# Optimization experiments

Measured on AMD Instinct MI355X. Metric: run time of the kernel, lower is better.

## Reference

```python
import jax, jax.numpy as jnp
import numpy as np

B, DIM, H, W = 8, 96, 256, 256
NH, WS, SS = 3, 8, 4
HD = DIM // NH
SCALE = HD ** -0.5
N = WS * WS  # tokens per window


def _rel_pos_log(ws):
    # [N, N, 2] signed log relative coordinates (matches get_relative_positions)
    coords = np.stack(np.meshgrid(np.arange(ws), np.arange(ws), indexing='ij'))
    cf = coords.reshape(2, -1)
    rel = (cf[:, :, None] - cf[:, None, :]).transpose(1, 2, 0).astype(np.float32)
    return np.sign(rel) * np.log1p(np.abs(rel))


def _attn_mask(Hh, Ww, ws, ss):
    # Swin shifted-window mask: [nW, N, N] with 0 / -100
    img = np.zeros((Hh, Ww))
    cnt = 0
    sl = (slice(0, -ws), slice(-ws, -ss), slice(-ss, None))
    for h in sl:
        for w in sl:
            img[h, w] = cnt
            cnt += 1
    mw = img.reshape(Hh // ws, ws, Ww // ws, ws).transpose(0, 2, 1, 3).reshape(-1, ws * ws)
    am = mw[:, None, :] - mw[:, :, None]
    return np.where(am != 0, -100.0, 0.0).astype(np.float32)


REL_POS = jnp.asarray(_rel_pos_log(WS))        # [N, N, 2]
ATTN_MASK = jnp.asarray(_attn_mask(H, W, WS, SS))  # [nW, N, N]


def setup_inputs() -> dict:
    key = jax.random.key(0)
    ks = jax.random.split(key, 8)
    s = 0.02
    return {
        'x': jax.random.normal(ks[0], (B, DIM, H, W), jnp.float32),
        'V_w': jax.random.normal(ks[1], (DIM, DIM), jnp.float32) * s,
        'V_b': jnp.zeros((DIM,), jnp.float32),
        'QK_w': jax.random.normal(ks[2], (2 * DIM, DIM), jnp.float32) * s,
        'QK_b': jnp.zeros((2 * DIM,), jnp.float32),
        'proj_w': jax.random.normal(ks[3], (DIM, DIM), jnp.float32) * s,
        'proj_b': jnp.zeros((DIM,), jnp.float32),
        'dw_w': jax.random.normal(ks[4], (DIM, 5, 5), jnp.float32) * s,
        'dw_b': jnp.zeros((DIM,), jnp.float32),
        'meta_w1': jax.random.normal(ks[5], (256, 2), jnp.float32) * 0.1,
        'meta_b1': jnp.zeros((256,), jnp.float32),
        'meta_w2': jax.random.normal(ks[6], (NH, 256), jnp.float32) * 0.1,
        'meta_b2': jnp.zeros((NH,), jnp.float32),
    }


def reference(x, V_w, V_b, QK_w, QK_b, proj_w, proj_b, dw_w, dw_b,
              meta_w1, meta_b1, meta_w2, meta_b2):
    # 1x1 convs as channel matmuls
    V = jnp.einsum('bchw,oc->bohw', x, V_w) + V_b[None, :, None, None]
    QK = jnp.einsum('bchw,oc->bohw', x, QK_w) + QK_b[None, :, None, None]
    qkv = jnp.concatenate([QK, V], axis=1).transpose(0, 2, 3, 1)  # [B,H,W,3C]
    # cyclic shift
    qkv = jnp.roll(qkv, (-SS, -SS), axis=(1, 2))
    # window partition -> [B*nW, N, 3C]
    xw = qkv.reshape(B, H // WS, WS, W // WS, WS, 3 * DIM)
    xw = xw.transpose(0, 1, 3, 2, 4, 5).reshape(-1, N, 3 * DIM)
    qkv3 = xw.reshape(-1, N, 3, NH, HD).transpose(2, 0, 3, 1, 4)  # [3, B_, nh, N, hd]
    q, k, v = qkv3[0] * SCALE, qkv3[1], qkv3[2]
    attn = jnp.einsum('whnd,whmd->whnm', q, k)  # [B_, nh, N, N]
    # MLP relative-position bias
    bias = jax.nn.relu(REL_POS @ meta_w1.T + meta_b1) @ meta_w2.T + meta_b2  # [N,N,nh]
    attn = attn + bias.transpose(2, 0, 1)[None]
    nW = ATTN_MASK.shape[0]
    attn = attn.reshape(B, nW, NH, N, N) + ATTN_MASK[None, :, None]
    attn = jax.nn.softmax(attn, axis=-1).reshape(-1, NH, N, N)
    xo = jnp.einsum('whnm,whmd->wnhd', attn, v).reshape(-1, N, DIM)
    # window reverse -> [B,H,W,C]
    xr = xo.reshape(B, H // WS, W // WS, WS, WS, DIM)
    xr = xr.transpose(0, 1, 3, 2, 4, 5).reshape(B, H, W, DIM)
    xr = jnp.roll(xr, (SS, SS), axis=(1, 2)).transpose(0, 3, 1, 2)  # [B,C,H,W]
    # depthwise 5x5 conv with reflect padding on V
    Vp = jnp.pad(V, ((0, 0), (0, 0), (2, 2), (2, 2)), mode='reflect')
    conv_out = jax.lax.conv_general_dilated(
        Vp, dw_w.reshape(DIM, 1, 5, 5), (1, 1), 'VALID',
        feature_group_count=DIM,
        dimension_numbers=('NCHW', 'OIHW', 'NCHW')) + dw_b[None, :, None, None]
    out = jnp.einsum('bchw,oc->bohw', conv_out + xr, proj_w) + proj_b[None, :, None, None]
    return out
```

## Files before the change

kernel.cpp:

```cpp
#include <hip/hip_runtime.h>
#include <hip/hip_bf16.h>

#define HW 65536
#define SCALE_Q 0.17677669529663687f

typedef __bf16 bf16x8 __attribute__((ext_vector_type(8)));
typedef float f32x4 __attribute__((ext_vector_type(4)));

__global__ void bias_kernel(const float* __restrict__ w1, const float* __restrict__ b1,
                            const float* __restrict__ w2, const float* __restrict__ b2,
                            float* __restrict__ biasF) {
    int gid = blockIdx.x * blockDim.x + threadIdx.x;
    if (gid >= 12288) return;
    int lane = gid & 63, r = (gid >> 6) & 3, ni = (gid >> 8) & 3, mi = (gid >> 10) & 3, h = gid >> 12;
    int i = mi * 16 + ((lane >> 4) << 2) + r;
    int j = ni * 16 + (lane & 15);
    float di = (float)((i >> 3) - (j >> 3));
    float dj = (float)((i & 7) - (j & 7));
    float r0 = (di > 0.f ? 1.f : (di < 0.f ? -1.f : 0.f)) * log1pf(fabsf(di));
    float r1 = (dj > 0.f ? 1.f : (dj < 0.f ? -1.f : 0.f)) * log1pf(fabsf(dj));
    float acc = 0.f;
    for (int t = 0; t < 256; ++t) {
        float u = fmaf(w1[2 * t], r0, fmaf(w1[2 * t + 1], r1, b1[t]));
        u = fmaxf(u, 0.f);
        acc = fmaf(w2[h * 256 + t], u, acc);
    }
    biasF[gid] = acc + b2[h];
}

__global__ void wtrans_kernel(const float* __restrict__ QK_w, const float* __restrict__ V_w,
                              const float* __restrict__ proj_w,
                              __bf16* __restrict__ Whi, __bf16* __restrict__ Wlo,
                              __bf16* __restrict__ WpHi, __bf16* __restrict__ WpLo) {
    int idx = blockIdx.x * blockDim.x + threadIdx.x;
    if (idx < 288 * 96) {
        int oo = idx / 96, c = idx - oo * 96;
        int h = oo / 96, rem = oo - h * 96, grp = rem >> 5, d = rem & 31;
        float w = (grp == 0) ? QK_w[(h * 32 + d) * 96 + c]
                : (grp == 1) ? QK_w[(96 + h * 32 + d) * 96 + c]
                             : V_w[(h * 32 + d) * 96 + c];
        __bf16 hi = (__bf16)w;
        Whi[idx] = hi;
        Wlo[idx] = (__bf16)(w - (float)hi);
    } else if (idx < 288 * 96 + 96 * 96) {
        int rdx = idx - 288 * 96;
        float w = proj_w[rdx];
        __bf16 hi = (__bf16)w;
        WpHi[rdx] = hi;
        WpLo[rdx] = (__bf16)(w - (float)hi);
    }
}

__global__ __launch_bounds__(256, 3) void fused_qkv_attn(
    const float* __restrict__ x,
    const __bf16* __restrict__ Whi, const __bf16* __restrict__ Wlo,
    const float* __restrict__ QK_b, const float* __restrict__ V_b,
    const float* __restrict__ biasF,
    unsigned short* __restrict__ Vout, float* __restrict__ xr) {
    __shared__ __align__(16) char lds[53376];
    int tid = threadIdx.x;
    int w4 = tid >> 6;
    int lane = tid & 63;
    int l16 = lane & 15;
    int g8 = (lane >> 4) << 3;
    int g4 = (lane >> 4) << 2;
    int bx0 = blockIdx.x;
    int bxs = (bx0 & 7) * 256 + (bx0 >> 3);
    int b = bxs >> 8;
    int wh = (bxs >> 3) & 31;
    int ww0 = (bxs & 7) << 2;
    int wh8 = wh << 3;
    int wb8 = ww0 << 3;
    int ww = ww0 + w4;
    int ti = lane >> 3, tj = lane & 7;
    int ph = (wh8 + ti + 4) & 255;
    int pw = ((ww << 3) + tj + 4) & 255;
    int pos   = ph * 256 + pw;
    int pos_s = (wh8 + ti) * 256 + (ww << 3) + tj;

    __bf16* Xh = (__bf16*)lds;
    const float* xb = x + (size_t)b * 96 * HW;
    for (int idx = tid; idx < 24576; idx += 256) {
        int c = idx >> 8, r = (idx >> 5) & 7, col = idx & 31;
        int pph = (wh8 + r + 4) & 255;
        int ppw = (wb8 + col + 4) & 255;
        Xh[(col >> 3) * 6672 + (r * 8 + (col & 7)) * 104 + c] =
            (__bf16)xb[(size_t)c * HW + pph * 256 + ppw];
    }
    __syncthreads();

    bf16x8 Ah[4][3];
    const __bf16* Xw = Xh + w4 * 6672;
#pragma unroll
    for (int mi = 0; mi < 4; ++mi)
#pragma unroll
        for (int ks = 0; ks < 3; ++ks)
            Ah[mi][ks] = *(const bf16x8*)(Xw + (mi * 16 + l16) * 104 + ks * 32 + g8);
    __syncthreads();

    char* hb = lds + w4 * 9984;
    __bf16* slab = (__bf16*)hb;
    __bf16* Vt   = (__bf16*)(hb + 5120);
    float*  Xr   = (float*)hb;

    bool bhh = (wh == 31), bww = (ww == 31);
    int rc[4];
#pragma unroll
    for (int ni = 0; ni < 4; ++ni) {
        int t = ni * 16 + l16;
        rc[ni] = (bhh ? (((t >> 3) < 4) ? 1 : 2) : 0) * 3 + (bww ? (((t & 7) < 4) ? 1 : 2) : 0);
    }

#pragma unroll 1
    for (int h = 0; h < 3; ++h) {
        bf16x8 Qf[4], Kf[4];
        {
            f32x4 acc[4][2];
#pragma unroll
            for (int mi = 0; mi < 4; ++mi)
#pragma unroll
                for (int ni = 0; ni < 2; ++ni) acc[mi][ni] = (f32x4){0.f, 0.f, 0.f, 0.f};
#pragma unroll
            for (int ks = 0; ks < 3; ++ks)
#pragma unroll
                for (int ni = 0; ni < 2; ++ni) {
                    bf16x8 Bh = *(const bf16x8*)(Whi + (h * 96 + ni * 16 + l16) * 96 + ks * 32 + g8);
#pragma unroll
                    for (int mi = 0; mi < 4; ++mi)
                        acc[mi][ni] = __builtin_amdgcn_mfma_f32_16x16x32_bf16(Ah[mi][ks], Bh, acc[mi][ni], 0, 0, 0);
                }
#pragma unroll
            for (int ni = 0; ni < 2; ++ni) {
                float bias = QK_b[h * 32 + ni * 16 + l16];
#pragma unroll
                for (int mi = 0; mi < 4; ++mi)
#pragma unroll
                    for (int r = 0; r < 4; ++r)
                        slab[(mi * 16 + g4 + r) * 40 + ni * 16 + l16] = (__bf16)((acc[mi][ni][r] + bias) * SCALE_Q);
            }
#pragma unroll
            for (int mi = 0; mi < 4; ++mi) Qf[mi] = *(const bf16x8*)(slab + (mi * 16 + l16) * 40 + g8);
        }
        {
            f32x4 acc[4][2];
#pragma unroll
            for (int mi = 0; mi < 4; ++mi)
#pragma unroll
                for (int ni = 0; ni < 2; ++ni) acc[mi][ni] = (f32x4){0.f, 0.f, 0.f, 0.f};
#pragma unroll
            for (int ks = 0; ks < 3; ++ks)
#pragma unroll
                for (int ni = 0; ni < 2; ++ni) {
                    bf16x8 Bh = *(const bf16x8*)(Whi + (h * 96 + 32 + ni * 16 + l16) * 96 + ks * 32 + g8);
#pragma unroll
                    for (int mi = 0; mi < 4; ++mi)
                        acc[mi][ni] = __builtin_amdgcn_mfma_f32_16x16x32_bf16(Ah[mi][ks], Bh, acc[mi][ni], 0, 0, 0);
                }
#pragma unroll
            for (int ni = 0; ni < 2; ++ni) {
                float bias = QK_b[96 + h * 32 + ni * 16 + l16];
#pragma unroll
                for (int mi = 0; mi < 4; ++mi)
#pragma unroll
                    for (int r = 0; r < 4; ++r)
                        slab[(mi * 16 + g4 + r) * 40 + ni * 16 + l16] = (__bf16)(acc[mi][ni][r] + bias);
            }
#pragma unroll
            for (int mi = 0; mi < 4; ++mi) Kf[mi] = *(const bf16x8*)(slab + (mi * 16 + l16) * 40 + g8);
        }
        {
            f32x4 acc[4][2];
#pragma unroll
            for (int mi = 0; mi < 4; ++mi)
#pragma unroll
                for (int ni = 0; ni < 2; ++ni) acc[mi][ni] = (f32x4){0.f, 0.f, 0.f, 0.f};
#pragma unroll
            for (int ks = 0; ks < 3; ++ks)
#pragma unroll
                for (int ni = 0; ni < 2; ++ni) {
                    int oo = (h * 96 + 64 + ni * 16 + l16) * 96 + ks * 32 + g8;
                    bf16x8 Bh = *(const bf16x8*)(Whi + oo);
                    bf16x8 Bl = *(const bf16x8*)(Wlo + oo);
#pragma unroll
                    for (int mi = 0; mi < 4; ++mi) {
                        acc[mi][ni] = __builtin_amdgcn_mfma_f32_16x16x32_bf16(Ah[mi][ks], Bh, acc[mi][ni], 0, 0, 0);
                        acc[mi][ni] = __builtin_amdgcn_mfma_f32_16x16x32_bf16(Ah[mi][ks], Bl, acc[mi][ni], 0, 0, 0);
                    }
                }
#pragma unroll
            for (int ni = 0; ni < 2; ++ni) {
                float bias = V_b[h * 32 + ni * 16 + l16];
#pragma unroll
                for (int mi = 0; mi < 4; ++mi)
#pragma unroll
                    for (int r = 0; r < 4; ++r)
                        Vt[(ni * 16 + l16) * 72 + mi * 16 + g4 + r] = (__bf16)(acc[mi][ni][r] + bias);
            }
        }
#pragma unroll
        for (int d = 0; d < 32; ++d)
            Vout[(size_t)(b * 96 + h * 32 + d) * HW + pos_s] = ((const unsigned short*)Vt)[d * 72 + lane];

        f32x4 sc[4][4];
#pragma unroll
        for (int mi = 0; mi < 4; ++mi)
#pragma unroll
            for (int ni = 0; ni < 4; ++ni) {
                sc[mi][ni] = (f32x4){0.f, 0.f, 0.f, 0.f};
                sc[mi][ni] = __builtin_amdgcn_mfma_f32_16x16x32_bf16(Qf[mi], Kf[ni], sc[mi][ni], 0, 0, 0);
            }
        const float* bF = biasF + h * 4096;
#pragma unroll
        for (int mi = 0; mi < 4; ++mi)
#pragma unroll
            for (int r = 0; r < 4; ++r) {
                int row = mi * 16 + g4 + r;
                float s0 = sc[mi][0][r] + bF[((mi * 4 + 0) * 4 + r) * 64 + lane];
                float s1 = sc[mi][1][r] + bF[((mi * 4 + 1) * 4 + r) * 64 + lane];
                float s2 = sc[mi][2][r] + bF[((mi * 4 + 2) * 4 + r) * 64 + lane];
                float s3 = sc[mi][3][r] + bF[((mi * 4 + 3) * 4 + r) * 64 + lane];
                if (bhh || bww) {
                    int rr = (bhh ? (((row >> 3) < 4) ? 1 : 2) : 0) * 3 +
                             (bww ? (((row & 7) < 4) ? 1 : 2) : 0);
                    if (rr != rc[0]) s0 -= 100.f;
                    if (rr != rc[1]) s1 -= 100.f;
                    if (rr != rc[2]) s2 -= 100.f;
                    if (rr != rc[3]) s3 -= 100.f;
                }
                float mm = fmaxf(fmaxf(s0, s1), fmaxf(s2, s3));
                mm = fmaxf(mm, __shfl_xor(mm, 1));
                mm = fmaxf(mm, __shfl_xor(mm, 2));
                mm = fmaxf(mm, __shfl_xor(mm, 4));
                mm = fmaxf(mm, __shfl_xor(mm, 8));
                float e0 = __expf(s0 - mm), e1 = __expf(s1 - mm);
                float e2 = __expf(s2 - mm), e3 = __expf(s3 - mm);
                float sum = e0 + e1 + e2 + e3;
                sum += __shfl_xor(sum, 1);
                sum += __shfl_xor(sum, 2);
                sum += __shfl_xor(sum, 4);
                sum += __shfl_xor(sum, 8);
                float inv = 1.f / sum;
                sc[mi][0][r] = e0 * inv;
                sc[mi][1][r] = e1 * inv;
                sc[mi][2][r] = e2 * inv;
                sc[mi][3][r] = e3 * inv;
            }
        f32x4 po[4][2];
#pragma unroll
        for (int mi = 0; mi < 4; ++mi)
#pragma unroll
            for (int ni = 0; ni < 2; ++ni) po[mi][ni] = (f32x4){0.f, 0.f, 0.f, 0.f};
#pragma unroll
        for (int ks = 0; ks < 2; ++ks) {
#pragma unroll
            for (int mi = 0; mi < 4; ++mi)
#pragma unroll
                for (int r = 0; r < 4; ++r) {
                    int row = mi * 16 + g4 + r;
                    slab[row * 40 + l16]      = (__bf16)sc[mi][ks * 2 + 0][r];
                    slab[row * 40 + 16 + l16] = (__bf16)sc[mi][ks * 2 + 1][r];
                }
            bf16x8 Vf[2], Pf;
#pragma unroll
            for (int ni = 0; ni < 2; ++ni)
                Vf[ni] = *(const bf16x8*)(Vt + (ni * 16 + l16) * 72 + ks * 32 + g8);
#pragma unroll
            for (int mi = 0; mi < 4; ++mi) {
                Pf = *(const bf16x8*)(slab + (mi * 16 + l16) * 40 + g8);
#pragma unroll
                for (int ni = 0; ni < 2; ++ni)
                    po[mi][ni] = __builtin_amdgcn_mfma_f32_16x16x32_bf16(Pf, Vf[ni], po[mi][ni], 0, 0, 0);
            }
        }
#pragma unroll
        for (int mi = 0; mi < 4; ++mi)
#pragma unroll
            for (int ni = 0; ni < 2; ++ni)
#pragma unroll
                for (int r = 0; r < 4; ++r)
                    Xr[(mi * 16 + g4 + r) * 36 + ni * 16 + l16] = po[mi][ni][r];
        float* xrg = xr + (size_t)(b * 96 + h * 32) * HW + pos;
#pragma unroll
        for (int c4 = 0; c4 < 8; ++c4) {
            f32x4 v = *(const f32x4*)(Xr + lane * 36 + c4 * 4);
            xrg[(size_t)(c4 * 4 + 0) * HW] = v[0];
            xrg[(size_t)(c4 * 4 + 1) * HW] = v[1];
            xrg[(size_t)(c4 * 4 + 2) * HW] = v[2];
            xrg[(size_t)(c4 * 4 + 3) * HW] = v[3];
        }
    }
}

__global__ __launch_bounds__(256) void dwproj_kernel(
    const __hip_bfloat16* __restrict__ Vs, const float* __restrict__ dw_w,
    const float* __restrict__ dw_b, const __bf16* __restrict__ WpHi,
    const __bf16* __restrict__ WpLo, const float* __restrict__ pb,
    float* __restrict__ T) {
    __shared__ __align__(16) __bf16 Ts[13312];
    int bx0 = blockIdx.x;
    int bx = (bx0 & 7) * 512 + (bx0 >> 3);
    int half = bx & 1, h = (bx >> 1) & 255, b = bx >> 9;
    int w0 = half << 7;
    int tid = threadIdx.x;
    for (int task = tid; task < 1536; task += 256) {
        int c = task >> 4, g = task & 15;
        int wbase = w0 + (g << 3);
        const __hip_bfloat16* Vp = Vs + (size_t)(b * 96 + c) * HW;
        const float* wt = dw_w + c * 25;
        float acc[8];
        float bias = dw_b[c];
#pragma unroll
        for (int i = 0; i < 8; ++i) acc[i] = bias;
        bool fast = (wbase >= 8) && (wbase <= 240);
#pragma unroll
        for (int dy = -2; dy <= 2; ++dy) {
            int hh = h + dy;
            hh = hh < 0 ? -hh : (hh > 255 ? 510 - hh : hh);
            int hs = (hh + 252) & 255;
            const __hip_bfloat16* row = Vp + hs * 256;
            float xv[12];
            if (fast) {
                const uint* rp = (const uint*)(row + (wbase - 6));
#pragma unroll
                for (int g2 = 0; g2 < 6; ++g2) {
                    uint u = rp[g2];
                    xv[2 * g2]     = __uint_as_float(u << 16);
                    xv[2 * g2 + 1] = __uint_as_float(u & 0xffff0000u);
                }
            } else {
#pragma unroll
                for (int idx = 0; idx < 12; ++idx) {
                    int cw = wbase - 2 + idx;
                    cw = cw < 0 ? -cw : (cw > 255 ? 510 - cw : cw);
                    int cs = (cw + 252) & 255;
                    uint u = *(const unsigned short*)(row + cs);
                    xv[idx] = __uint_as_float(u << 16);
                }
            }
            const float* w5 = wt + (dy + 2) * 5;
#pragma unroll
            for (int dx = 0; dx < 5; ++dx) {
                float wv = w5[dx];
#pragma unroll
                for (int i = 0; i < 8; ++i) acc[i] = fmaf(wv, xv[i + dx], acc[i]);
            }
        }
        const float* xp = T + (size_t)(b * 96 + c) * HW + h * 256;
        f32x4 x0 = *(const f32x4*)(xp + wbase);
        f32x4 x1 = *(const f32x4*)(xp + wbase + 4);
#pragma unroll
        for (int i = 0; i < 4; ++i) { acc[i] += x0[i]; acc[4 + i] += x1[i]; }
#pragma unroll
        for (int i = 0; i < 8; ++i) Ts[(g * 8 + i) * 104 + c] = (__bf16)acc[i];
    }
    __syncthreads();
    int lane = tid & 63;
    int l16 = lane & 15;
    int g8 = (lane >> 4) << 3;
    int g4 = (lane >> 4) << 2;
    int wv = tid >> 6;
    f32x4 po[2][6];
#pragma unroll
    for (int mi = 0; mi < 2; ++mi)
#pragma unroll
        for (int ni = 0; ni < 6; ++ni) po[mi][ni] = (f32x4){0.f, 0.f, 0.f, 0.f};
#pragma unroll
    for (int ks = 0; ks < 3; ++ks) {
        bf16x8 Av[2];
#pragma unroll
        for (int mi = 0; mi < 2; ++mi)
            Av[mi] = *(const bf16x8*)(Ts + (wv * 32 + mi * 16 + l16) * 104 + ks * 32 + g8);
#pragma unroll
        for (int ni = 0; ni < 6; ++ni) {
            int o = ni * 16 + l16;
            bf16x8 Bh = *(const bf16x8*)(WpHi + o * 96 + ks * 32 + g8);
            bf16x8 Bl = *(const bf16x8*)(WpLo + o * 96 + ks * 32 + g8);
#pragma unroll
            for (int mi = 0; mi < 2; ++mi) {
                po[mi][ni] = __builtin_amdgcn_mfma_f32_16x16x32_bf16(Av[mi], Bh, po[mi][ni], 0, 0, 0);
                po[mi][ni] = __builtin_amdgcn_mfma_f32_16x16x32_bf16(Av[mi], Bl, po[mi][ni], 0, 0, 0);
            }
        }
    }
#pragma unroll
    for (int ni = 0; ni < 6; ++ni) {
        int o = ni * 16 + l16;
        float bias = pb[o];
#pragma unroll
        for (int mi = 0; mi < 2; ++mi) {
            f32x4 v = po[mi][ni];
            v[0] += bias; v[1] += bias; v[2] += bias; v[3] += bias;
            *(f32x4*)(T + (size_t)(b * 96 + o) * HW + h * 256 + w0 + wv * 32 + mi * 16 + g4) = v;
        }
    }
}

extern "C" void kernel_launch(void* const* d_in, const int* in_sizes, int n_in,
                              void* d_out, int out_size, void* d_ws, size_t ws_size,
                              hipStream_t stream) {
    const float* x      = (const float*)d_in[0];
    const float* V_w    = (const float*)d_in[1];
    const float* V_b    = (const float*)d_in[2];
    const float* QK_w   = (const float*)d_in[3];
    const float* QK_b   = (const float*)d_in[4];
    const float* proj_w = (const float*)d_in[5];
    const float* proj_b = (const float*)d_in[6];
    const float* dw_w   = (const float*)d_in[7];
    const float* dw_b   = (const float*)d_in[8];
    const float* mw1    = (const float*)d_in[9];
    const float* mb1    = (const float*)d_in[10];
    const float* mw2    = (const float*)d_in[11];
    const float* mb2    = (const float*)d_in[12];
    float* out = (float*)d_out;

    char* ws = (char*)d_ws;
    __hip_bfloat16* Vbuf = (__hip_bfloat16*)ws;
    float*  biasF = (float*)(ws + 100663296);
    __bf16* Whi   = (__bf16*)(ws + 100663296 + 49152);
    __bf16* Wlo   = (__bf16*)(ws + 100663296 + 49152 + 55296);
    __bf16* WpHi  = (__bf16*)(ws + 100663296 + 49152 + 2 * 55296);
    __bf16* WpLo  = (__bf16*)(ws + 100663296 + 49152 + 2 * 55296 + 18432);

    bias_kernel<<<48, 256, 0, stream>>>(mw1, mb1, mw2, mb2, biasF);
    wtrans_kernel<<<144, 256, 0, stream>>>(QK_w, V_w, proj_w, Whi, Wlo, WpHi, WpLo);
    fused_qkv_attn<<<2048, 256, 0, stream>>>(x, Whi, Wlo, QK_b, V_b, biasF,
                                             (unsigned short*)Vbuf, out);
    dwproj_kernel<<<4096, 256, 0, stream>>>(Vbuf, dw_w, dw_b, WpHi, WpLo, proj_b, out);
}
```

Baseline: 710.5 us.

## Store attention output intermediate as bf16 and raise wave priority around MFMA blocks

The attention kernel now writes its windowed output to a separate bf16 workspace buffer instead of fp32 into the output tensor, and the depthwise/projection kernel reads it back as packed bf16. This halves the traffic for that intermediate in both the write and the read. It also wraps MFMA loops in s_setprio to favour matrix issue. It costs extra precision loss on the attention branch. The bf16 path is only taken when the workspace is large enough.

```diff
diff --git a/kernel.cpp b/kernel.cpp
--- a/kernel.cpp
+++ b/kernel.cpp
@@ -51,12 +51,13 @@
     }
 }
 
+template <bool XRB>
 __global__ __launch_bounds__(256, 3) void fused_qkv_attn(
     const float* __restrict__ x,
     const __bf16* __restrict__ Whi, const __bf16* __restrict__ Wlo,
     const float* __restrict__ QK_b, const float* __restrict__ V_b,
     const float* __restrict__ biasF,
-    unsigned short* __restrict__ Vout, float* __restrict__ xr) {
+    unsigned short* __restrict__ Vout, void* __restrict__ xrv) {
     __shared__ __align__(16) char lds[53376];
     int tid = threadIdx.x;
     int w4 = tid >> 6;
@@ -120,6 +121,7 @@
             for (int mi = 0; mi < 4; ++mi)
 #pragma unroll
                 for (int ni = 0; ni < 2; ++ni) acc[mi][ni] = (f32x4){0.f, 0.f, 0.f, 0.f};
+            __builtin_amdgcn_s_setprio(1);
 #pragma unroll
             for (int ks = 0; ks < 3; ++ks)
 #pragma unroll
@@ -129,6 +131,7 @@
                     for (int mi = 0; mi < 4; ++mi)
                         acc[mi][ni] = __builtin_amdgcn_mfma_f32_16x16x32_bf16(Ah[mi][ks], Bh, acc[mi][ni], 0, 0, 0);
                 }
+            __builtin_amdgcn_s_setprio(0);
 #pragma unroll
             for (int ni = 0; ni < 2; ++ni) {
                 float bias = QK_b[h * 32 + ni * 16 + l16];
@@ -147,6 +150,7 @@
             for (int mi = 0; mi < 4; ++mi)
 #pragma unroll
                 for (int ni = 0; ni < 2; ++ni) acc[mi][ni] = (f32x4){0.f, 0.f, 0.f, 0.f};
+            __builtin_amdgcn_s_setprio(1);
 #pragma unroll
             for (int ks = 0; ks < 3; ++ks)
 #pragma unroll
@@ -156,6 +160,7 @@
                     for (int mi = 0; mi < 4; ++mi)
                         acc[mi][ni] = __builtin_amdgcn_mfma_f32_16x16x32_bf16(Ah[mi][ks], Bh, acc[mi][ni], 0, 0, 0);
                 }
+            __builtin_amdgcn_s_setprio(0);
 #pragma unroll
             for (int ni = 0; ni < 2; ++ni) {
                 float bias = QK_b[96 + h * 32 + ni * 16 + l16];
@@ -174,6 +179,7 @@
             for (int mi = 0; mi < 4; ++mi)
 #pragma unroll
                 for (int ni = 0; ni < 2; ++ni) acc[mi][ni] = (f32x4){0.f, 0.f, 0.f, 0.f};
+            __builtin_amdgcn_s_setprio(1);
 #pragma unroll
             for (int ks = 0; ks < 3; ++ks)
 #pragma unroll
@@ -187,6 +193,7 @@
                         acc[mi][ni] = __builtin_amdgcn_mfma_f32_16x16x32_bf16(Ah[mi][ks], Bl, acc[mi][ni], 0, 0, 0);
                     }
                 }
+            __builtin_amdgcn_s_setprio(0);
 #pragma unroll
             for (int ni = 0; ni < 2; ++ni) {
                 float bias = V_b[h * 32 + ni * 16 + l16];
@@ -202,6 +209,7 @@
             Vout[(size_t)(b * 96 + h * 32 + d) * HW + pos_s] = ((const unsigned short*)Vt)[d * 72 + lane];
 
         f32x4 sc[4][4];
+        __builtin_amdgcn_s_setprio(1);
 #pragma unroll
         for (int mi = 0; mi < 4; ++mi)
 #pragma unroll
@@ -209,6 +217,7 @@
                 sc[mi][ni] = (f32x4){0.f, 0.f, 0.f, 0.f};
                 sc[mi][ni] = __builtin_amdgcn_mfma_f32_16x16x32_bf16(Qf[mi], Kf[ni], sc[mi][ni], 0, 0, 0);
             }
+        __builtin_amdgcn_s_setprio(0);
         const float* bF = biasF + h * 4096;
 #pragma unroll
         for (int mi = 0; mi < 4; ++mi)
@@ -264,6 +273,7 @@
 #pragma unroll
             for (int ni = 0; ni < 2; ++ni)
                 Vf[ni] = *(const bf16x8*)(Vt + (ni * 16 + l16) * 72 + ks * 32 + g8);
+            __builtin_amdgcn_s_setprio(1);
 #pragma unroll
             for (int mi = 0; mi < 4; ++mi) {
                 Pf = *(const bf16x8*)(slab + (mi * 16 + l16) * 40 + g8);
@@ -271,6 +281,7 @@
                 for (int ni = 0; ni < 2; ++ni)
                     po[mi][ni] = __builtin_amdgcn_mfma_f32_16x16x32_bf16(Pf, Vf[ni], po[mi][ni], 0, 0, 0);
             }
+            __builtin_amdgcn_s_setprio(0);
         }
 #pragma unroll
         for (int mi = 0; mi < 4; ++mi)
@@ -279,23 +290,37 @@
 #pragma unroll
                 for (int r = 0; r < 4; ++r)
                     Xr[(mi * 16 + g4 + r) * 36 + ni * 16 + l16] = po[mi][ni][r];
-        float* xrg = xr + (size_t)(b * 96 + h * 32) * HW + pos;
-#pragma unroll
-        for (int c4 = 0; c4 < 8; ++c4) {
-            f32x4 v = *(const f32x4*)(Xr + lane * 36 + c4 * 4);
-            xrg[(size_t)(c4 * 4 + 0) * HW] = v[0];
-            xrg[(size_t)(c4 * 4 + 1) * HW] = v[1];
-            xrg[(size_t)(c4 * 4 + 2) * HW] = v[2];
-            xrg[(size_t)(c4 * 4 + 3) * HW] = v[3];
+        if constexpr (XRB) {
+            unsigned short* xrg = (unsigned short*)xrv + (size_t)(b * 96 + h * 32) * HW + pos;
+#pragma unroll
+            for (int c4 = 0; c4 < 8; ++c4) {
+                f32x4 v = *(const f32x4*)(Xr + lane * 36 + c4 * 4);
+#pragma unroll
+                for (int j = 0; j < 4; ++j) {
+                    __bf16 t = (__bf16)v[j];
+                    xrg[(size_t)(c4 * 4 + j) * HW] = *(unsigned short*)&t;
+                }
+            }
+        } else {
+            float* xrg = (float*)xrv + (size_t)(b * 96 + h * 32) * HW + pos;
+#pragma unroll
+            for (int c4 = 0; c4 < 8; ++c4) {
+                f32x4 v = *(const f32x4*)(Xr + lane * 36 + c4 * 4);
+                xrg[(size_t)(c4 * 4 + 0) * HW] = v[0];
+                xrg[(size_t)(c4 * 4 + 1) * HW] = v[1];
+                xrg[(size_t)(c4 * 4 + 2) * HW] = v[2];
+                xrg[(size_t)(c4 * 4 + 3) * HW] = v[3];
+            }
         }
     }
 }
 
+template <bool XRB>
 __global__ __launch_bounds__(256) void dwproj_kernel(
     const __hip_bfloat16* __restrict__ Vs, const float* __restrict__ dw_w,
     const float* __restrict__ dw_b, const __bf16* __restrict__ WpHi,
     const __bf16* __restrict__ WpLo, const float* __restrict__ pb,
-    float* __restrict__ T) {
+    const void* __restrict__ xrv, float* __restrict__ T) {
     __shared__ __align__(16) __bf16 Ts[13312];
     int bx0 = blockIdx.x;
     int bx = (bx0 & 7) * 512 + (bx0 >> 3);
@@ -345,11 +370,24 @@
                 for (int i = 0; i < 8; ++i) acc[i] = fmaf(wv, xv[i + dx], acc[i]);
             }
         }
-        const float* xp = T + (size_t)(b * 96 + c) * HW + h * 256;
-        f32x4 x0 = *(const f32x4*)(xp + wbase);
-        f32x4 x1 = *(const f32x4*)(xp + wbase + 4);
-#pragma unroll
-        for (int i = 0; i < 4; ++i) { acc[i] += x0[i]; acc[4 + i] += x1[i]; }
+        if constexpr (XRB) {
+            const unsigned short* xp = (const unsigned short*)xrv + (size_t)(b * 96 + c) * HW + h * 256 + wbase;
+            uint4 u = *(const uint4*)xp;
+            acc[0] += __uint_as_float(u.x << 16);
+            acc[1] += __uint_as_float(u.x & 0xffff0000u);
+            acc[2] += __uint_as_float(u.y << 16);
+            acc[3] += __uint_as_float(u.y & 0xffff0000u);
+            acc[4] += __uint_as_float(u.z << 16);
+            acc[5] += __uint_as_float(u.z & 0xffff0000u);
+            acc[6] += __uint_as_float(u.w << 16);
+            acc[7] += __uint_as_float(u.w & 0xffff0000u);
+        } else {
+            const float* xp = (const float*)xrv + (size_t)(b * 96 + c) * HW + h * 256;
+            f32x4 x0 = *(const f32x4*)(xp + wbase);
+            f32x4 x1 = *(const f32x4*)(xp + wbase + 4);
+#pragma unroll
+            for (int i = 0; i < 4; ++i) { acc[i] += x0[i]; acc[4 + i] += x1[i]; }
+        }
 #pragma unroll
         for (int i = 0; i < 8; ++i) Ts[(g * 8 + i) * 104 + c] = (__bf16)acc[i];
     }
@@ -414,16 +452,30 @@
     float* out = (float*)d_out;
 
     char* ws = (char*)d_ws;
+    const size_t VB = 100663296;
+    bool xrb = (ws_size >= 2 * VB + 49152 + 2 * 55296 + 2 * 18432);
+
     __hip_bfloat16* Vbuf = (__hip_bfloat16*)ws;
-    float*  biasF = (float*)(ws + 100663296);
-    __bf16* Whi   = (__bf16*)(ws + 100663296 + 49152);
-    __bf16* Wlo   = (__bf16*)(ws + 100663296 + 49152 + 55296);
-    __bf16* WpHi  = (__bf16*)(ws + 100663296 + 49152 + 2 * 55296);
-    __bf16* WpLo  = (__bf16*)(ws + 100663296 + 49152 + 2 * 55296 + 18432);
+    size_t off = VB;
+    unsigned short* xr16 = nullptr;
+    if (xrb) { xr16 = (unsigned short*)(ws + off); off += VB; }
+    float*  biasF = (float*)(ws + off); off += 49152;
+    __bf16* Whi   = (__bf16*)(ws + off); off += 55296;
+    __bf16* Wlo   = (__bf16*)(ws + off); off += 55296;
+    __bf16* WpHi  = (__bf16*)(ws + off); off += 18432;
+    __bf16* WpLo  = (__bf16*)(ws + off);
 
     bias_kernel<<<48, 256, 0, stream>>>(mw1, mb1, mw2, mb2, biasF);
     wtrans_kernel<<<144, 256, 0, stream>>>(QK_w, V_w, proj_w, Whi, Wlo, WpHi, WpLo);
-    fused_qkv_attn<<<2048, 256, 0, stream>>>(x, Whi, Wlo, QK_b, V_b, biasF,
-                                             (unsigned short*)Vbuf, out);
-    dwproj_kernel<<<4096, 256, 0, stream>>>(Vbuf, dw_w, dw_b, WpHi, WpLo, proj_b, out);
+    if (xrb) {
+        fused_qkv_attn<true><<<2048, 256, 0, stream>>>(x, Whi, Wlo, QK_b, V_b, biasF,
+                                                       (unsigned short*)Vbuf, (void*)xr16);
+        dwproj_kernel<true><<<4096, 256, 0, stream>>>(Vbuf, dw_w, dw_b, WpHi, WpLo, proj_b,
+                                                      (const void*)xr16, out);
+    } else {
+        fused_qkv_attn<false><<<2048, 256, 0, stream>>>(x, Whi, Wlo, QK_b, V_b, biasF,
+                                                        (unsigned short*)Vbuf, (void*)out);
+        dwproj_kernel<false><<<4096, 256, 0, stream>>>(Vbuf, dw_w, dw_b, WpHi, WpLo, proj_b,
+                                                       (const void*)out, out);
+    }
 }
```

Result: faster. 683.5 us (-3.8%).
